# Kernel optimization log

Hardware: AMD Instinct MI355X
Metric: run time of the kernel (lower is better)

Reference implementation:

```python
import jax, jax.numpy as jnp
import numpy as np

B, S, E = 2, 2048, 2048
H, W = 16, 256  # num_heads, window_size
D = E // H      # head_dim = 128


def setup_inputs() -> dict:
    key = jax.random.key(0)
    ks = jax.random.split(key, 9)
    s = 1.0 / np.sqrt(E)
    return {
        "x": jax.random.normal(ks[0], (B, S, E), dtype=jnp.float32),
        "Wq": jax.random.normal(ks[1], (E, E), dtype=jnp.float32) * s,
        "bq": jax.random.normal(ks[2], (E,), dtype=jnp.float32) * 0.01,
        "Wk": jax.random.normal(ks[3], (E, E), dtype=jnp.float32) * s,
        "bk": jax.random.normal(ks[4], (E,), dtype=jnp.float32) * 0.01,
        "Wv": jax.random.normal(ks[5], (E, E), dtype=jnp.float32) * s,
        "bv": jax.random.normal(ks[6], (E,), dtype=jnp.float32) * 0.01,
        "Wo": jax.random.normal(ks[7], (E, E), dtype=jnp.float32) * s,
        "bo": jax.random.normal(ks[8], (E,), dtype=jnp.float32) * 0.01,
    }


def reference(x, Wq, bq, Wk, bk, Wv, bv, Wo, bo):
    Bsz, Sl, _ = x.shape
    # projections -> [B, H, S, D]
    def proj(Wt, bt):
        return (x @ Wt + bt).reshape(Bsz, Sl, H, D).transpose(0, 2, 1, 3)
    q = proj(Wq, bq)
    k = proj(Wk, bk)
    v = proj(Wv, bv)
    # scores [B, H, S, S]
    scores = jnp.einsum("bhqd,bhkd->bhqk", q, k) / jnp.sqrt(jnp.float32(D))
    # causal sliding-window mask: q_pos - W < k_pos <= q_pos
    q_pos = jnp.arange(Sl)[:, None]
    k_pos = jnp.arange(Sl)[None, :]
    valid = (k_pos <= q_pos) & (k_pos > q_pos - W)
    scores = jnp.where(valid, scores, jnp.float32(-jnp.inf))
    attn = jax.nn.softmax(scores, axis=-1)
    ctx = jnp.einsum("bhqk,bhkd->bhqd", attn, v)
    ctx = ctx.transpose(0, 2, 1, 3).reshape(Bsz, Sl, E)
    out = ctx @ Wo + bo
    return out, k, v
```

## Files before the change

kernel.cpp:

```cpp
#include <hip/hip_runtime.h>
#include <hip/hip_bf16.h>

#define SEQ 2048
#define EMB 2048
#define NH 16
#define WIN 256
#define HD 128
#define KDIM 2048
#define NDIM 2048

typedef __bf16 bf16x8 __attribute__((ext_vector_type(8)));
typedef float f32x4 __attribute__((ext_vector_type(4)));

__device__ __forceinline__ ushort f2bf(float f) {
  unsigned int x = __float_as_uint(f);
  unsigned int r = (x + 0x7fffu + ((x >> 16) & 1u)) >> 16;
  return (ushort)r;
}

__global__ __launch_bounds__(256) void wtrans_kernel(
    const float* __restrict__ w0, const float* __restrict__ w1,
    const float* __restrict__ w2, const float* __restrict__ w3,
    ushort* __restrict__ wt) {
  __shared__ __align__(16) float tf[32 * 132];
  const int t = threadIdx.x;
  const int nblk = blockIdx.x, kblk = blockIdx.y, mat = blockIdx.z;
  const float* Wp = mat == 0 ? w0 : mat == 1 ? w1 : mat == 2 ? w2 : w3;
  const int n0 = nblk * 128, k0 = kblk * 32;
#pragma unroll
  for (int p = 0; p < 4; ++p) {
    int kk = (t >> 5) + 8 * p;
    int nn = (t & 31) * 4;
    float4 v = *(const float4*)&Wp[(size_t)(k0 + kk) * NDIM + n0 + nn];
    *(float4*)&tf[kk * 132 + nn] = v;
  }
  __syncthreads();
  ushort* dst = wt + (size_t)mat * ((size_t)NDIM * KDIM) +
                (size_t)(nblk * 64 + kblk) * 4096;
#pragma unroll
  for (int p = 0; p < 2; ++p) {
    int idx = p * 256 + t;
    int r = idx >> 2, cs = idx & 3;
    int c = cs ^ ((r >> 1) & 3);
    union { ushort u[8]; uint4 v; } pk;
#pragma unroll
    for (int j = 0; j < 8; ++j) pk.u[j] = f2bf(tf[(c * 8 + j) * 132 + r]);
    *(uint4*)&dst[idx * 8] = pk.v;
  }
}

template <int MODE>
__global__ __launch_bounds__(256) void gemm_kernel(
    const void* __restrict__ Aptr, const ushort* __restrict__ Wt,
    const float* __restrict__ b0, const float* __restrict__ b1,
    const float* __restrict__ b2, float* __restrict__ outF,
    ushort* __restrict__ outQ) {
  __shared__ __align__(16) ushort As[128 * 32];
  __shared__ __align__(16) ushort Bs[128 * 32];
  const int t = threadIdx.x;
  const int mblk = blockIdx.x, nblk = blockIdx.y, z = blockIdx.z;
  const int m0 = mblk * 128, n0 = nblk * 128;
  const ushort* wtile = Wt + (size_t)z * ((size_t)NDIM * KDIM) +
                        (size_t)(nblk * 64) * 4096;
  const int lane = t & 63, wid = t >> 6;
  const int l15 = lane & 15, lg = lane >> 4;
  const int wm = wid >> 1, wn = wid & 1;
  f32x4 acc[4][4] = {};

  for (int kt = 0; kt < KDIM / 32; ++kt) {
    __syncthreads();
    {
      const uint4* src = (const uint4*)(wtile + (size_t)kt * 4096);
#pragma unroll
      for (int p = 0; p < 2; ++p) {
        int idx = p * 256 + t;
        *(uint4*)&Bs[idx * 8] = src[idx];
      }
    }
#pragma unroll
    for (int p = 0; p < 2; ++p) {
      int r = (t >> 2) + 64 * p;
      int cs = t & 3;
      int c = cs ^ ((r >> 1) & 3);
      union { ushort u[8]; uint4 v; } pk;
      if (MODE == 1) {
        const float* ap = (const float*)Aptr + (size_t)(m0 + r) * KDIM + kt * 32 + c * 8;
        float4 f0 = *(const float4*)ap;
        float4 f1 = *(const float4*)(ap + 4);
        pk.u[0] = f2bf(f0.x); pk.u[1] = f2bf(f0.y);
        pk.u[2] = f2bf(f0.z); pk.u[3] = f2bf(f0.w);
        pk.u[4] = f2bf(f1.x); pk.u[5] = f2bf(f1.y);
        pk.u[6] = f2bf(f1.z); pk.u[7] = f2bf(f1.w);
      } else {
        pk.v = *(const uint4*)((const ushort*)Aptr + (size_t)(m0 + r) * KDIM + kt * 32 + c * 8);
      }
      *(uint4*)&As[r * 32 + cs * 8] = pk.v;
    }
    __syncthreads();
    bf16x8 af[4], bfr[4];
#pragma unroll
    for (int mf = 0; mf < 4; ++mf) {
      int r = wm * 64 + mf * 16 + l15;
      af[mf] = *(const bf16x8*)&As[r * 32 + ((lg ^ ((r >> 1) & 3)) * 8)];
    }
#pragma unroll
    for (int nf = 0; nf < 4; ++nf) {
      int r = wn * 64 + nf * 16 + l15;
      bfr[nf] = *(const bf16x8*)&Bs[r * 32 + ((lg ^ ((r >> 1) & 3)) * 8)];
    }
#pragma unroll
    for (int mf = 0; mf < 4; ++mf)
#pragma unroll
      for (int nf = 0; nf < 4; ++nf)
        acc[mf][nf] = __builtin_amdgcn_mfma_f32_16x16x32_bf16(
            af[mf], bfr[nf], acc[mf][nf], 0, 0, 0);
  }

  const float* bias = (MODE == 0) ? b0 : (z == 0 ? b0 : z == 1 ? b1 : b2);
#pragma unroll
  for (int nf = 0; nf < 4; ++nf) {
    int nl = wn * 64 + nf * 16 + l15;
    int n = n0 + nl;
    float bv = bias[n];
#pragma unroll
    for (int mf = 0; mf < 4; ++mf) {
#pragma unroll
      for (int r = 0; r < 4; ++r) {
        int m = m0 + wm * 64 + mf * 16 + lg * 4 + r;
        float val = acc[mf][nf][r] + bv;
        if (MODE == 0) {
          outF[(size_t)m * NDIM + n] = val;
        } else {
          int b = m >> 11, s = m & 2047;
          size_t idx = (((size_t)b * NH + nblk) * SEQ + s) * HD + nl;
          if (z == 0) outQ[idx] = f2bf(val);
          else outF[(z == 1 ? 8388608u : 16777216u) + idx] = val;
        }
      }
    }
  }
}

__global__ __launch_bounds__(256) void attn_kernel(
    const ushort* __restrict__ Qb, const float* __restrict__ Kf,
    const float* __restrict__ Vf, ushort* __restrict__ ctx) {
  __shared__ __align__(16) ushort Kl[64 * 128];
  __shared__ __align__(16) ushort Vl[128 * 72];
  __shared__ __align__(16) ushort Pl[4 * 16 * 72];
  const int t = threadIdx.x;
  const int bh = blockIdx.x;
  const int q0 = blockIdx.y * 64;
  const int lane = t & 63, w = t >> 6;
  const int l15 = lane & 15, lg = lane >> 4;
  const int b = bh >> 4, h = bh & 15;
  const ushort* Qbase = Qb + (size_t)bh * SEQ * HD;
  const float* Kbase = Kf + (size_t)bh * SEQ * HD;
  const float* Vbase = Vf + (size_t)bh * SEQ * HD;

  bf16x8 aq[4];
#pragma unroll
  for (int ds = 0; ds < 4; ++ds)
    aq[ds] = *(const bf16x8*)&Qbase[(size_t)(q0 + w * 16 + l15) * HD + ds * 32 + lg * 8];

  f32x4 accc[8] = {};
  float mrow[4], lrow[4];
#pragma unroll
  for (int r = 0; r < 4; ++r) { mrow[r] = -1e30f; lrow[r] = 0.f; }

  int ktlo = (q0 - WIN + 1) >> 6;
  if (ktlo < 0) ktlo = 0;
  const int kthi = q0 >> 6;

  for (int kt = ktlo; kt <= kthi; ++kt) {
    __syncthreads();
#pragma unroll
    for (int p = 0; p < 4; ++p) {
      int idx = p * 256 + t;
      int row = idx >> 4, cs = idx & 15;
      int c = cs ^ (row & 7);
      const float* sp = &Kbase[(size_t)(kt * 64 + row) * HD + c * 8];
      float4 f0 = *(const float4*)sp;
      float4 f1 = *(const float4*)(sp + 4);
      union { ushort u[8]; uint4 v; } pk;
      pk.u[0] = f2bf(f0.x); pk.u[1] = f2bf(f0.y);
      pk.u[2] = f2bf(f0.z); pk.u[3] = f2bf(f0.w);
      pk.u[4] = f2bf(f1.x); pk.u[5] = f2bf(f1.y);
      pk.u[6] = f2bf(f1.z); pk.u[7] = f2bf(f1.w);
      *(uint4*)&Kl[row * 128 + cs * 8] = pk.v;
    }
#pragma unroll
    for (int p = 0; p < 4; ++p) {
      int idx = p * 256 + t;
      int key = idx & 63, dc = idx >> 6;
      const float* sp = &Vbase[(size_t)(kt * 64 + key) * HD + dc * 8];
      float4 f0 = *(const float4*)sp;
      float4 f1 = *(const float4*)(sp + 4);
      Vl[(dc * 8 + 0) * 72 + key] = f2bf(f0.x);
      Vl[(dc * 8 + 1) * 72 + key] = f2bf(f0.y);
      Vl[(dc * 8 + 2) * 72 + key] = f2bf(f0.z);
      Vl[(dc * 8 + 3) * 72 + key] = f2bf(f0.w);
      Vl[(dc * 8 + 4) * 72 + key] = f2bf(f1.x);
      Vl[(dc * 8 + 5) * 72 + key] = f2bf(f1.y);
      Vl[(dc * 8 + 6) * 72 + key] = f2bf(f1.z);
      Vl[(dc * 8 + 7) * 72 + key] = f2bf(f1.w);
    }
    __syncthreads();

    f32x4 sacc[4] = {};
#pragma unroll
    for (int ds = 0; ds < 4; ++ds) {
#pragma unroll
      for (int kf = 0; kf < 4; ++kf) {
        int key = kf * 16 + l15;
        bf16x8 kb = *(const bf16x8*)&Kl[key * 128 + (((ds * 4 + lg) ^ (key & 7)) * 8)];
        sacc[kf] = __builtin_amdgcn_mfma_f32_16x16x32_bf16(aq[ds], kb, sacc[kf], 0, 0, 0);
      }
    }

    const float scale = 0.08838834764831845f;
    const float L2E = 1.4426950408889634f;
#pragma unroll
    for (int r = 0; r < 4; ++r) {
      int q = q0 + w * 16 + lg * 4 + r;
      float sv[4];
      float mx = -1e30f;
#pragma unroll
      for (int kf = 0; kf < 4; ++kf) {
        int key = kt * 64 + kf * 16 + l15;
        float s = sacc[kf][r] * scale;
        bool valid = (key <= q) && (key + WIN > q);
        s = valid ? s : -1e30f;
        sv[kf] = s;
        mx = fmaxf(mx, s);
      }
      mx = fmaxf(mx, __shfl_xor(mx, 1));
      mx = fmaxf(mx, __shfl_xor(mx, 2));
      mx = fmaxf(mx, __shfl_xor(mx, 4));
      mx = fmaxf(mx, __shfl_xor(mx, 8));
      float mnew = fmaxf(mrow[r], mx);
      float sf = exp2f((mrow[r] - mnew) * L2E);
      float ps = 0.f;
#pragma unroll
      for (int kf = 0; kf < 4; ++kf) {
        float p = (sv[kf] > -1e29f) ? exp2f((sv[kf] - mnew) * L2E) : 0.f;
        ps += p;
        Pl[w * 1152 + (lg * 4 + r) * 72 + kf * 16 + l15] = f2bf(p);
      }
      ps += __shfl_xor(ps, 1);
      ps += __shfl_xor(ps, 2);
      ps += __shfl_xor(ps, 4);
      ps += __shfl_xor(ps, 8);
      lrow[r] = lrow[r] * sf + ps;
      mrow[r] = mnew;
#pragma unroll
      for (int nf = 0; nf < 8; ++nf) accc[nf][r] *= sf;
    }

#pragma unroll
    for (int ks = 0; ks < 2; ++ks) {
      bf16x8 pa = *(const bf16x8*)&Pl[w * 1152 + l15 * 72 + ks * 32 + lg * 8];
#pragma unroll
      for (int nf = 0; nf < 8; ++nf) {
        bf16x8 vb = *(const bf16x8*)&Vl[(nf * 16 + l15) * 72 + ks * 32 + lg * 8];
        accc[nf] = __builtin_amdgcn_mfma_f32_16x16x32_bf16(pa, vb, accc[nf], 0, 0, 0);
      }
    }
  }

#pragma unroll
  for (int r = 0; r < 4; ++r) {
    int q = q0 + w * 16 + lg * 4 + r;
    float inv = 1.0f / lrow[r];
    size_t rowoff = ((size_t)b * SEQ + q) * EMB + (size_t)h * HD;
#pragma unroll
    for (int nf = 0; nf < 8; ++nf)
      ctx[rowoff + nf * 16 + l15] = f2bf(accc[nf][r] * inv);
  }
}

extern "C" void kernel_launch(void* const* d_in, const int* in_sizes, int n_in,
                              void* d_out, int out_size, void* d_ws, size_t ws_size,
                              hipStream_t stream) {
  const float* x  = (const float*)d_in[0];
  const float* Wq = (const float*)d_in[1];
  const float* bq = (const float*)d_in[2];
  const float* Wk = (const float*)d_in[3];
  const float* bk = (const float*)d_in[4];
  const float* Wv = (const float*)d_in[5];
  const float* bv = (const float*)d_in[6];
  const float* Wo = (const float*)d_in[7];
  const float* bo = (const float*)d_in[8];
  float* out = (float*)d_out;
  ushort* ws = (ushort*)d_ws;
  ushort* Wt  = ws;
  ushort* Qb  = ws + 16777216;
  ushort* ctxb = ws + 25165824;

  wtrans_kernel<<<dim3(16, 64, 4), 256, 0, stream>>>(Wq, Wk, Wv, Wo, Wt);
  gemm_kernel<1><<<dim3(32, 16, 3), 256, 0, stream>>>(x, Wt, bq, bk, bv, out, Qb);
  attn_kernel<<<dim3(32, 32), 256, 0, stream>>>(Qb, out + 8388608, out + 16777216, ctxb);
  gemm_kernel<0><<<dim3(32, 16, 1), 256, 0, stream>>>(ctxb, Wt + (size_t)3 * 4194304,
                                                      bo, nullptr, nullptr, out, nullptr);
}
```

Measured before the change: 281.3 us.

## Pre-convert x to bf16 and load GEMM tiles via direct global-to-LDS loads

Adds a separate kernel that converts the fp32 input x to bf16 once, so the QKV GEMM no longer converts x on every tile load, and it reads half the bytes per A element. The GEMM tile staging for A and B is replaced with global_load_lds 16-byte direct-to-LDS transfers, which skip the register round trip. Each lane's source address is precomputed with the XOR swizzle, so the LDS layout matches the previous one. The cost is an extra launch and an extra pass over x, and the bf16 copy of x reuses the ctx workspace buffer.

```diff
diff --git a/kernel.cpp b/kernel.cpp
--- a/kernel.cpp
+++ b/kernel.cpp
@@ -16,6 +16,25 @@
   unsigned int x = __float_as_uint(f);
   unsigned int r = (x + 0x7fffu + ((x >> 16) & 1u)) >> 16;
   return (ushort)r;
+}
+
+__device__ __forceinline__ void gl16(const ushort* g, ushort* l) {
+  __builtin_amdgcn_global_load_lds(
+      (const __attribute__((address_space(1))) ushort*)g,
+      (__attribute__((address_space(3))) ushort*)l, 16, 0, 0);
+}
+
+__global__ __launch_bounds__(256) void xconv_kernel(
+    const float* __restrict__ x, ushort* __restrict__ xb) {
+  size_t i = ((size_t)blockIdx.x * 256 + threadIdx.x) * 8;
+  float4 f0 = *(const float4*)&x[i];
+  float4 f1 = *(const float4*)&x[i + 4];
+  union { ushort u[8]; uint4 v; } pk;
+  pk.u[0] = f2bf(f0.x); pk.u[1] = f2bf(f0.y);
+  pk.u[2] = f2bf(f0.z); pk.u[3] = f2bf(f0.w);
+  pk.u[4] = f2bf(f1.x); pk.u[5] = f2bf(f1.y);
+  pk.u[6] = f2bf(f1.z); pk.u[7] = f2bf(f1.w);
+  *(uint4*)&xb[i] = pk.v;
 }
 
 __global__ __launch_bounds__(256) void wtrans_kernel(
@@ -51,7 +70,7 @@
 
 template <int MODE>
 __global__ __launch_bounds__(256) void gemm_kernel(
-    const void* __restrict__ Aptr, const ushort* __restrict__ Wt,
+    const ushort* __restrict__ Ab, const ushort* __restrict__ Wt,
     const float* __restrict__ b0, const float* __restrict__ b1,
     const float* __restrict__ b2, float* __restrict__ outF,
     ushort* __restrict__ outQ) {
@@ -67,35 +86,24 @@
   const int wm = wid >> 1, wn = wid & 1;
   f32x4 acc[4][4] = {};
 
+  const int slot0 = wid * 128 + lane;
+  const int slot1 = slot0 + 64;
+  const int r0 = slot0 >> 2, c0 = (slot0 & 3) ^ ((r0 >> 1) & 3);
+  const int r1 = slot1 >> 2, c1 = (slot1 & 3) ^ ((r1 >> 1) & 3);
+  const ushort* aS0 = Ab + (size_t)(m0 + r0) * KDIM + c0 * 8;
+  const ushort* aS1 = Ab + (size_t)(m0 + r1) * KDIM + c1 * 8;
+  const ushort* bS0 = wtile + slot0 * 8;
+  const ushort* bS1 = wtile + slot1 * 8;
+  ushort* aD0 = &As[(wid * 128) * 8];
+  ushort* aD1 = &As[(wid * 128 + 64) * 8];
+  ushort* bD0 = &Bs[(wid * 128) * 8];
+  ushort* bD1 = &Bs[(wid * 128 + 64) * 8];
+
   for (int kt = 0; kt < KDIM / 32; ++kt) {
     __syncthreads();
-    {
-      const uint4* src = (const uint4*)(wtile + (size_t)kt * 4096);
-#pragma unroll
-      for (int p = 0; p < 2; ++p) {
-        int idx = p * 256 + t;
-        *(uint4*)&Bs[idx * 8] = src[idx];
-      }
-    }
-#pragma unroll
-    for (int p = 0; p < 2; ++p) {
-      int r = (t >> 2) + 64 * p;
-      int cs = t & 3;
-      int c = cs ^ ((r >> 1) & 3);
-      union { ushort u[8]; uint4 v; } pk;
-      if (MODE == 1) {
-        const float* ap = (const float*)Aptr + (size_t)(m0 + r) * KDIM + kt * 32 + c * 8;
-        float4 f0 = *(const float4*)ap;
-        float4 f1 = *(const float4*)(ap + 4);
-        pk.u[0] = f2bf(f0.x); pk.u[1] = f2bf(f0.y);
-        pk.u[2] = f2bf(f0.z); pk.u[3] = f2bf(f0.w);
-        pk.u[4] = f2bf(f1.x); pk.u[5] = f2bf(f1.y);
-        pk.u[6] = f2bf(f1.z); pk.u[7] = f2bf(f1.w);
-      } else {
-        pk.v = *(const uint4*)((const ushort*)Aptr + (size_t)(m0 + r) * KDIM + kt * 32 + c * 8);
-      }
-      *(uint4*)&As[r * 32 + cs * 8] = pk.v;
-    }
+    gl16(aS0, aD0); gl16(aS1, aD1);
+    gl16(bS0, bD0); gl16(bS1, bD1);
+    aS0 += 32; aS1 += 32; bS0 += 4096; bS1 += 4096;
     __syncthreads();
     bf16x8 af[4], bfr[4];
 #pragma unroll
@@ -292,12 +300,14 @@
   const float* bo = (const float*)d_in[8];
   float* out = (float*)d_out;
   ushort* ws = (ushort*)d_ws;
-  ushort* Wt  = ws;
-  ushort* Qb  = ws + 16777216;
-  ushort* ctxb = ws + 25165824;
-
+  ushort* Wt   = ws;
+  ushort* Qb   = ws + 16777216;
+  ushort* xb   = ws + 25165824;
+  ushort* ctxb = xb;
+
+  xconv_kernel<<<4096, 256, 0, stream>>>(x, xb);
   wtrans_kernel<<<dim3(16, 64, 4), 256, 0, stream>>>(Wq, Wk, Wv, Wo, Wt);
-  gemm_kernel<1><<<dim3(32, 16, 3), 256, 0, stream>>>(x, Wt, bq, bk, bv, out, Qb);
+  gemm_kernel<1><<<dim3(32, 16, 3), 256, 0, stream>>>(xb, Wt, bq, bk, bv, out, Qb);
   attn_kernel<<<dim3(32, 32), 256, 0, stream>>>(Qb, out + 8388608, out + 16777216, ctxb);
   gemm_kernel<0><<<dim3(32, 16, 1), 256, 0, stream>>>(ctxb, Wt + (size_t)3 * 4194304,
                                                       bo, nullptr, nullptr, out, nullptr);
```

New measurement: 236.6 us. 1.19x faster.
